# Kernel tuning notes

Hardware: AMD Instinct MI355X
Metric: run time of the kernel (lower is better)

Reference implementation:

```python
import jax, jax.numpy as jnp
import numpy as np

B, NS, NT = 8, 1024, 1024
SRC, TGT, OUT, H = 1024, 1024, 1024, 8
DH = OUT // H  # per-head dim = 128


def setup_inputs() -> dict:
    key = jax.random.key(0)
    ks = jax.random.split(key, 9)
    s = 0.02
    return {
        "src": jax.random.normal(ks[0], (B, NS, SRC), jnp.float32),
        "tgt": jax.random.normal(ks[1], (B, NT, TGT), jnp.float32),
        "src_mask": jnp.ones((B, NS), jnp.float32),
        "tgt_mask": jnp.ones((B, NT), jnp.float32),
        "Ws": jax.random.normal(ks[2], (2 * OUT, SRC), jnp.float32) * s,
        "bs": jnp.zeros((2 * OUT,), jnp.float32),
        "Wt": jax.random.normal(ks[3], (OUT, TGT), jnp.float32) * s,
        "bt": jnp.zeros((OUT,), jnp.float32),
        "Wo": jax.random.normal(ks[4], (OUT, OUT + TGT), jnp.float32) * s,
        "bo": jnp.zeros((OUT,), jnp.float32),
    }


def reference(src, tgt, src_mask, tgt_mask, Ws, bs, Wt, bt, Wo, bo):
    # src_lin / tgt_lin (FCNet = linear, no activation, drop=0 at eval)
    src_trans = jnp.einsum("bsf,of->bso", src, Ws) + bs  # [B,NS,2*OUT]
    tgt_trans = jnp.einsum("btf,of->bto", tgt, Wt) + bt  # [B,NT,OUT]
    src_trans = src_trans * src_mask[:, :, None]
    tgt_trans = tgt_trans * tgt_mask[:, :, None]

    src_key, src_val = jnp.split(src_trans, 2, axis=2)  # each [B,NS,OUT]
    # head split along channels == reshape to [.., H, DH]
    k = src_key.reshape(B, NS, H, DH)
    v = src_val.reshape(B, NS, H, DH)
    q = tgt_trans.reshape(B, NT, H, DH)

    scores = jnp.einsum("bthd,bshd->bhts", q, k) / jnp.sqrt(jnp.float32(DH))
    scores = jnp.where(src_mask[:, None, None, :] == 0, -jnp.inf, scores)
    attn = jax.nn.softmax(scores, axis=-1)  # [B,H,NT,NS]
    tgt_update = jnp.einsum("bhts,bshd->bthd", attn, v).reshape(B, NT, OUT)

    cat_tgt = jnp.concatenate([tgt, tgt_update], axis=2)  # [B,NT,TGT+OUT]
    update_tgt = jnp.einsum("btf,of->bto", cat_tgt, Wo) + bo
    return update_tgt
```

## Files before the change

kernel.cpp:

```cpp
#include <hip/hip_runtime.h>


typedef __bf16 bf16x8 __attribute__((ext_vector_type(8)));
typedef float f32x4 __attribute__((ext_vector_type(4)));
typedef unsigned short u16;
typedef unsigned short u16x8 __attribute__((ext_vector_type(8)));

#define MFMA16(a, b, c) __builtin_amdgcn_mfma_f32_16x16x32_bf16((a), (b), (c), 0, 0, 0)

__device__ __forceinline__ float bf2f(u16 b) {
  return __uint_as_float(((unsigned)b) << 16);
}
__device__ __forceinline__ u16 f2bf(float f) {
  unsigned u = __float_as_uint(f);
  u += 0x7fffu + ((u >> 16) & 1u);
  return (u16)(u >> 16);
}
__device__ __forceinline__ u16 f2bf_hw(float f) {
  __bf16 h = (__bf16)f;
  return __builtin_bit_cast(u16, h);
}

__device__ __forceinline__ void async16(const u16* g, u16* l) {
  __builtin_amdgcn_global_load_lds(
      (const __attribute__((address_space(1))) unsigned int*)g,
      (__attribute__((address_space(3))) unsigned int*)l, 16, 0, 0);
}

struct Cvt5 {
  const float* src[5];
  unsigned cnt4[5];
  unsigned ooff[5];
};

__global__ __launch_bounds__(256)
void cvt5_kernel(Cvt5 a, u16* __restrict__ out, unsigned total4)
{
  unsigned gid = blockIdx.x * 256u + threadIdx.x;
  if (gid >= total4) return;
  unsigned rem = gid;
  int s = 0;
  while (s < 4 && rem >= a.cnt4[s]) { rem -= a.cnt4[s]; ++s; }
  const float4 v = ((const float4*)a.src[s])[rem];
  ushort4 o;
  o.x = f2bf(v.x); o.y = f2bf(v.y); o.z = f2bf(v.z); o.w = f2bf(v.w);
  *(ushort4*)(out + a.ooff[s] + (size_t)rem * 4) = o;
}

__global__ __launch_bounds__(256, 3)
void gemm12_kernel(const u16* __restrict__ srcb, const u16* __restrict__ tgtb,
                   const u16* __restrict__ Wsb, const u16* __restrict__ Wtb,
                   const float* __restrict__ bs, const float* __restrict__ bt,
                   const float* __restrict__ smask, const float* __restrict__ tmask,
                   u16* __restrict__ kvbuf, u16* __restrict__ qbuf)
{
  __shared__ u16 smem[16384];
  u16* As = smem;
  u16* Bs = smem + 8192;

  const int tid  = threadIdx.x;
  const int lane = tid & 63;
  const int w    = tid >> 6;
  const int wm = w >> 1, wn = w & 1;
  const int quad = lane >> 4, lr = lane & 15;

  const unsigned nwg  = gridDim.x * gridDim.y;
  const unsigned wgid = blockIdx.y * gridDim.x + blockIdx.x;
  const unsigned swz  = (wgid & 7u) * (nwg >> 3) + (wgid >> 3);
  const int nt = (int)(swz % gridDim.x);
  const int mt = (int)(swz / gridDim.x);
  const int m0 = mt * 128;
  const int n0 = nt * 128;

  const bool isQ = (n0 >= 2048);
  const u16* Ap = isQ ? tgtb : srcb;
  const u16* Bp = isQ ? (Wtb + (size_t)(n0 - 2048) * 1024)
                      : (Wsb + (size_t)n0 * 1024);
  const float* bias = isQ ? (bt + (n0 - 2048)) : (bs + n0);
  const float* rsc  = isQ ? tmask : smask;

  const f32x4 z4 = {0.f, 0.f, 0.f, 0.f};
  f32x4 acc[4][4];
#pragma unroll
  for (int i = 0; i < 4; ++i)
#pragma unroll
    for (int j = 0; j < 4; ++j)
      acc[i][j] = z4;

  const int acolsw = (((tid & 7) ^ ((tid >> 3) & 7)) * 8);
  const int ssw = lr & 7;

  for (int k0 = 0; k0 < 1024; k0 += 64) {
    __syncthreads();
#pragma unroll
    for (int it = 0; it < 4; ++it) {
      const int row = it * 32 + (tid >> 3);
      const int ldsbase = (it * 256 + (tid & 192)) * 8;
      async16(Ap + (size_t)(m0 + row) * 1024 + (k0 + acolsw), &As[ldsbase]);
      async16(Bp + (size_t)row * 1024        + (k0 + acolsw), &Bs[ldsbase]);
    }
    __syncthreads();

#pragma unroll
    for (int kk = 0; kk < 2; ++kk) {
      const int rc = (((kk << 2) | quad) ^ ssw) * 8;
      bf16x8 af[4], bfr[4];
#pragma unroll
      for (int i = 0; i < 4; ++i)
        af[i] = *(const bf16x8*)&As[(wm * 64 + i * 16 + lr) * 64 + rc];
#pragma unroll
      for (int j = 0; j < 4; ++j)
        bfr[j] = *(const bf16x8*)&Bs[(wn * 64 + j * 16 + lr) * 64 + rc];
#pragma unroll
      for (int i = 0; i < 4; ++i)
#pragma unroll
        for (int j = 0; j < 4; ++j)
          acc[i][j] = MFMA16(af[i], bfr[j], acc[i][j]);
    }
  }

  float bv[4];
#pragma unroll
  for (int j = 0; j < 4; ++j)
    bv[j] = bias[wn * 64 + j * 16 + lr];

  if (isQ) {
    const int c0 = n0 - 2048;
#pragma unroll
    for (int i = 0; i < 4; ++i)
#pragma unroll
      for (int r = 0; r < 4; ++r) {
        const int grow = m0 + wm * 64 + i * 16 + quad * 4 + r;
        const float rs = rsc[grow];
#pragma unroll
        for (int j = 0; j < 4; ++j) {
          const int gcol = c0 + wn * 64 + j * 16 + lr;
          qbuf[(size_t)grow * 1024 + gcol] = f2bf_hw((acc[i][j][r] + bv[j]) * rs);
        }
      }
  } else {
    u16* kvtile = smem;
    __syncthreads();

    const int bb  = m0 >> 10;
    const int s0b = m0 & 1023;
    const bool isK = (n0 < 1024);
    const int h = (isK ? n0 : n0 - 1024) >> 7;
    const size_t bh = (size_t)(bb * 8 + h);

#pragma unroll
    for (int i = 0; i < 4; ++i)
#pragma unroll
      for (int r = 0; r < 4; ++r) {
        const int sl = wm * 64 + i * 16 + quad * 4 + r;
        const float rs = rsc[m0 + sl];
#pragma unroll
        for (int j = 0; j < 4; ++j) {
          const int d = wn * 64 + j * 16 + lr;
          const float val = (acc[i][j][r] + bv[j]) * rs;
          int c, e;
          if (isK) {
            c = (d >> 3) * 128 + sl;
            c ^= ((c >> 2) & 2) ^ ((c >> 7) & 1);
            e = d & 7;
          } else {
            c = (sl >> 6) * 1024 + (((sl >> 3) & 7) * 128) + d;
            c ^= (c >> 7) & 1;
            e = sl & 7;
          }
          kvtile[c * 8 + e] = f2bf_hw(val);
        }
      }
    __syncthreads();

    const size_t gbase = isK
        ? (bh * 131072 + (size_t)s0b * 8)
        : ((size_t)8388608 + bh * 131072 + (size_t)(s0b >> 6) * 8192);
#pragma unroll
    for (int it = 0; it < 8; ++it) {
      const int idx = it * 256 + tid;
      int lc;
      size_t dst;
      if (isK) {
        lc  = idx ^ ((idx >> 2) & 2) ^ ((idx >> 7) & 1);
        dst = gbase + (size_t)(idx >> 7) * 8192 + (size_t)(idx & 127) * 8;
      } else {
        lc  = idx ^ ((idx >> 7) & 1);
        dst = gbase + (size_t)idx * 8;
      }
      *(u16x8*)(kvbuf + dst) = *(const u16x8*)&kvtile[lc * 8];
    }
  }
}

__global__ __launch_bounds__(256, 3)
void gemm3_kernel(const u16* __restrict__ A0, const u16* __restrict__ A1,
                  const u16* __restrict__ Bw, const float* __restrict__ bias,
                  float* __restrict__ C)
{
  __shared__ u16 As[128 * 64];
  __shared__ u16 Bs[128 * 64];
  const int tid  = threadIdx.x;
  const int lane = tid & 63;
  const int w    = tid >> 6;
  const int wm = w >> 1, wn = w & 1;
  const int quad = lane >> 4, lr = lane & 15;
  const unsigned nwg  = gridDim.x * gridDim.y;
  const unsigned wgid = blockIdx.y * gridDim.x + blockIdx.x;
  const unsigned swz  = (wgid & 7u) * (nwg >> 3) + (wgid >> 3);
  const int m0 = (int)(swz / gridDim.x) * 128;
  const int n0 = (int)(swz % gridDim.x) * 128;

  const f32x4 z4 = {0.f, 0.f, 0.f, 0.f};
  f32x4 acc[4][4];
#pragma unroll
  for (int i = 0; i < 4; ++i)
#pragma unroll
    for (int j = 0; j < 4; ++j)
      acc[i][j] = z4;

  const int acolsw = (((tid & 7) ^ ((tid >> 3) & 7)) * 8);
  const int ssw = lr & 7;

  auto kstep = [&](const u16* Ap, int kk0, int k0) {
    __syncthreads();
#pragma unroll
    for (int it = 0; it < 4; ++it) {
      const int row = it * 32 + (tid >> 3);
      const int ldsbase = (it * 256 + (tid & 192)) * 8;
      async16(Ap + (size_t)(m0 + row) * 1024 + (kk0 + acolsw), &As[ldsbase]);
      async16(Bw + (size_t)(n0 + row) * 2048 + (k0 + acolsw), &Bs[ldsbase]);
    }
    __syncthreads();

#pragma unroll
    for (int kk = 0; kk < 2; ++kk) {
      const int rc = (((kk << 2) | quad) ^ ssw) * 8;
      bf16x8 af[4], bfr[4];
#pragma unroll
      for (int i = 0; i < 4; ++i)
        af[i] = *(const bf16x8*)&As[(wm * 64 + i * 16 + lr) * 64 + rc];
#pragma unroll
      for (int j = 0; j < 4; ++j)
        bfr[j] = *(const bf16x8*)&Bs[(wn * 64 + j * 16 + lr) * 64 + rc];
#pragma unroll
      for (int i = 0; i < 4; ++i)
#pragma unroll
        for (int j = 0; j < 4; ++j)
          acc[i][j] = MFMA16(af[i], bfr[j], acc[i][j]);
    }
  };

  for (int k0 = 0; k0 < 1024; k0 += 64) kstep(A0, k0, k0);
  for (int k0 = 1024; k0 < 2048; k0 += 64) kstep(A1, k0 - 1024, k0);

  float bv[4];
#pragma unroll
  for (int j = 0; j < 4; ++j)
    bv[j] = bias[n0 + wn * 64 + j * 16 + lr];

#pragma unroll
  for (int i = 0; i < 4; ++i)
#pragma unroll
    for (int r = 0; r < 4; ++r) {
      const int grow = m0 + wm * 64 + i * 16 + quad * 4 + r;
#pragma unroll
      for (int j = 0; j < 4; ++j) {
        const int gcol = n0 + wn * 64 + j * 16 + lr;
        C[(size_t)grow * 1024 + gcol] = acc[i][j][r] + bv[j];
      }
    }
}

#define SCLOG2E 0.12751813754618667f

__global__ __launch_bounds__(256, 2)
void flash_kernel(const u16* __restrict__ q, const u16* __restrict__ Kg,
                  const u16* __restrict__ Vg,
                  const float* __restrict__ smask, u16* __restrict__ upd)
{
  __shared__ u16 Ks[2][64 * 128];
  __shared__ u16 Vs[2][64 * 128];
  __shared__ u16 Ps[4][2 * 16 * 64];

  const int tid  = threadIdx.x;
  const int lane = tid & 63;
  const int w    = tid >> 6;
  const int quad = lane >> 4, lr = lane & 15;
  const int bh_i = blockIdx.x;
  const int qt   = blockIdx.y;
  const int b = bh_i >> 3, h = bh_i & 7;
  const size_t bh = (size_t)bh_i;

  const size_t qrow0 = (size_t)b * 1024 + qt * 128 + w * 16;

  bf16x8 qf[2][4];
#pragma unroll
  for (int s = 0; s < 2; ++s)
#pragma unroll
    for (int kk = 0; kk < 4; ++kk)
      qf[s][kk] = *(const bf16x8*)
          &q[(qrow0 + s * 64 + lr) * 1024 + h * 128 + kk * 32 + quad * 8];

  unsigned long long mbits = 0ull;
#pragma unroll
  for (int t = 0; t < 16; ++t)
#pragma unroll
    for (int j = 0; j < 4; ++j) {
      const float mv = smask[b * 1024 + t * 64 + j * 16 + lr];
      if (mv == 0.f) mbits |= (1ull << (t * 4 + j));
    }

  auto stage = [&](int t, int bb) {
    const int s0 = t * 64;
#pragma unroll
    for (int it = 0; it < 4; ++it) {
      const int dc = it * 4 + w;
      async16(Kg + (((bh * 16 + dc) * 1024) + s0 + lane) * 8,
              &Ks[bb][(it * 256 + (tid & 192)) * 8]);
    }
#pragma unroll
    for (int it = 0; it < 4; ++it) {
      async16(Vg + ((bh * 16 + t) * 1024 + it * 256 + tid) * 8,
              &Vs[bb][(it * 256 + (tid & 192)) * 8]);
    }
  };

  const f32x4 z4 = {0.f, 0.f, 0.f, 0.f};
  f32x4 oacc[2][8];
#pragma unroll
  for (int s = 0; s < 2; ++s)
#pragma unroll
    for (int jd = 0; jd < 8; ++jd) oacc[s][jd] = z4;
  float lsum[2][4] = {{0.f, 0.f, 0.f, 0.f}, {0.f, 0.f, 0.f, 0.f}};

  stage(0, 0);
  stage(1, 1);

#pragma unroll 1
  for (int t = 0; t < 16; ++t) {
    const int bb = t & 1;
    asm volatile("s_waitcnt vmcnt(8)" ::: "memory");
    __builtin_amdgcn_s_barrier();

    float mb[4];
#pragma unroll
    for (int j = 0; j < 4; ++j)
      mb[j] = ((mbits >> (t * 4 + j)) & 1ull) ? -1e30f : 0.f;

    f32x4 sacc[2][4];
#pragma unroll
    for (int s = 0; s < 2; ++s)
#pragma unroll
      for (int j = 0; j < 4; ++j) sacc[s][j] = z4;
    __builtin_amdgcn_s_setprio(1);
#pragma unroll
    for (int kk = 0; kk < 4; ++kk) {
      bf16x8 kb[4];
#pragma unroll
      for (int j = 0; j < 4; ++j)
        kb[j] = *(const bf16x8*)&Ks[bb][((kk * 4 + quad) * 64 + j * 16 + lr) * 8];
#pragma unroll
      for (int s = 0; s < 2; ++s)
#pragma unroll
        for (int j = 0; j < 4; ++j)
          sacc[s][j] = MFMA16(qf[s][kk], kb[j], sacc[s][j]);
    }
    __builtin_amdgcn_s_setprio(0);

#pragma unroll
    for (int s = 0; s < 2; ++s)
#pragma unroll
      for (int r = 0; r < 4; ++r) {
        const int row = quad * 4 + r;
        const int rsw = (row & 7) * 8;
        float ps = 0.f;
#pragma unroll
        for (int j = 0; j < 4; ++j) {
          const float p = exp2f(fmaf(sacc[s][j][r], SCLOG2E, mb[j]));
          ps += p;
          Ps[w][s * 1024 + row * 64 + ((j * 16 + lr) ^ rsw)] = f2bf_hw(p);
        }
        lsum[s][r] += ps;
      }

    __builtin_amdgcn_s_setprio(1);
#pragma unroll
    for (int kk2 = 0; kk2 < 2; ++kk2) {
      bf16x8 pa[2], vb[8];
#pragma unroll
      for (int s = 0; s < 2; ++s)
        pa[s] = *(const bf16x8*)
            &Ps[w][s * 1024 + lr * 64 + ((kk2 * 32 + quad * 8) ^ ((lr & 7) * 8))];
#pragma unroll
      for (int jd = 0; jd < 8; ++jd)
        vb[jd] = *(const bf16x8*)&Vs[bb][((kk2 * 4 + quad) * 128 + jd * 16 + lr) * 8];
#pragma unroll
      for (int s = 0; s < 2; ++s)
#pragma unroll
        for (int jd = 0; jd < 8; ++jd)
          oacc[s][jd] = MFMA16(pa[s], vb[jd], oacc[s][jd]);
    }
    __builtin_amdgcn_s_setprio(0);

    __builtin_amdgcn_s_barrier();
    stage((t + 2) & 15, bb);
  }

  asm volatile("s_waitcnt vmcnt(0)" ::: "memory");

#pragma unroll
  for (int s = 0; s < 2; ++s)
#pragma unroll
    for (int r = 0; r < 4; ++r) {
      float l = lsum[s][r];
      l += __shfl_xor(l, 1);
      l += __shfl_xor(l, 2);
      l += __shfl_xor(l, 4);
      l += __shfl_xor(l, 8);
      const float inv = 1.f / l;
      const size_t grow = qrow0 + s * 64 + quad * 4 + r;
#pragma unroll
      for (int jd = 0; jd < 8; ++jd)
        upd[grow * 1024 + h * 128 + jd * 16 + lr] = f2bf_hw(oacc[s][jd][r] * inv);
    }
}

__global__ void magic_kernel(float* out, float val)
{
  if (threadIdx.x == 0 && blockIdx.x == 0) out[0] = val;
}

extern "C" void kernel_launch(void* const* d_in, const int* in_sizes, int n_in,
                              void* d_out, int out_size, void* d_ws, size_t ws_size,
                              hipStream_t stream)
{
  static const int dict_sz[10]   = {8388608, 8388608, 8192, 8192, 2097152,
                                    2048, 1048576, 1024, 2097152, 1024};
  static const int sorted_sz[10] = {2097152, 2097152, 1048576, 1024, 2048,
                                    1024, 8388608, 8192, 8388608, 8192};
  bool is_dict = (n_in == 10), is_sorted = (n_in == 10);
  if (n_in == 10) {
    for (int i = 0; i < 10; ++i) {
      if (in_sizes[i] != dict_sz[i])   is_dict = false;
      if (in_sizes[i] != sorted_sz[i]) is_sorted = false;
    }
  }

  const float *src, *tgt, *smask, *tmask, *Ws, *bs, *Wt, *bt, *Wo, *bo;
  if (is_sorted) {
    Wo    = (const float*)d_in[0];
    Ws    = (const float*)d_in[1];
    Wt    = (const float*)d_in[2];
    bo    = (const float*)d_in[3];
    bs    = (const float*)d_in[4];
    bt    = (const float*)d_in[5];
    src   = (const float*)d_in[6];
    smask = (const float*)d_in[7];
    tgt   = (const float*)d_in[8];
    tmask = (const float*)d_in[9];
  } else {
    src   = (const float*)d_in[0];
    tgt   = (const float*)d_in[1];
    smask = (const float*)d_in[2];
    tmask = (const float*)d_in[3];
    Ws    = (const float*)d_in[4];
    bs    = (const float*)d_in[5];
    Wt    = (const float*)d_in[6];
    bt    = (const float*)d_in[7];
    Wo    = (const float*)d_in[8];
    bo    = (const float*)d_in[9];
  }
  float* out = (float*)d_out;

  const size_t KV = 16777216, Q = 8388608, UPD = 8388608;
  const unsigned segsz[5] = {8388608u, 8388608u, 2097152u, 1048576u, 2097152u};
  size_t total_u16 = KV + Q + UPD;
  unsigned aoff[5], off = 0, total4 = 0;
  for (int i = 0; i < 5; ++i) {
    aoff[i] = off;
    off += segsz[i];
    total4 += segsz[i] / 4u;
  }
  total_u16 += off;

  unsigned ws_mb = (unsigned)(ws_size >> 20);
  if (ws_mb > 999u) ws_mb = 999u;
  if (!is_dict && !is_sorted) {
    magic_kernel<<<dim3(1), dim3(64), 0, stream>>>(out, 4000.f + (float)ws_mb);
    return;
  }
  if (ws_size < total_u16 * 2) {
    magic_kernel<<<dim3(1), dim3(64), 0, stream>>>(out, 3000.f + (float)ws_mb);
    return;
  }

  u16* kvbuf  = (u16*)d_ws;
  u16* qbuf   = kvbuf + KV;
  u16* updbuf = qbuf + Q;
  u16* arena  = updbuf + UPD;

  Cvt5 ca;
  const float* segp[5] = {src, tgt, Ws, Wt, Wo};
  for (int i = 0; i < 5; ++i) {
    ca.src[i]  = segp[i];
    ca.cnt4[i] = segsz[i] / 4u;
    ca.ooff[i] = aoff[i];
  }
  const u16* srcb = arena + aoff[0];
  const u16* tgtb = arena + aoff[1];
  const u16* Wsb  = arena + aoff[2];
  const u16* Wtb  = arena + aoff[3];
  const u16* Wob  = arena + aoff[4];

  dim3 blk(256);
  cvt5_kernel<<<dim3((total4 + 255u) / 256u), blk, 0, stream>>>(ca, arena, total4);
  gemm12_kernel<<<dim3(24, 64), blk, 0, stream>>>(
      srcb, tgtb, Wsb, Wtb, bs, bt, smask, tmask, kvbuf, qbuf);
  flash_kernel<<<dim3(64, 8), blk, 0, stream>>>(
      qbuf, kvbuf, kvbuf + 8388608, smask, updbuf);
  gemm3_kernel<<<dim3(8, 64), blk, 0, stream>>>(
      tgtb, updbuf, Wob, bo, out);
}
```

Measured before the change: 300.8 us.

## Overlap tgt half of output GEMM with attention in one heterogeneous launch

```diff
diff --git a/kernel.cpp b/kernel.cpp
--- a/kernel.cpp
+++ b/kernel.cpp
@@ -193,10 +193,236 @@
   }
 }
 
+#define SCLOG2E 0.12751813754618667f
+
+__global__ __launch_bounds__(256, 2)
+void fused_fg_kernel(const u16* __restrict__ q, const u16* __restrict__ Kg,
+                     const u16* __restrict__ Vg, const float* __restrict__ smask,
+                     u16* __restrict__ upd,
+                     const u16* __restrict__ tgtb, const u16* __restrict__ Wob,
+                     const float* __restrict__ bo, float* __restrict__ out)
+{
+  __shared__ u16 smem[40960];
+  const int tid  = threadIdx.x;
+  const int lane = tid & 63;
+  const int w    = tid >> 6;
+  const int quad = lane >> 4, lr = lane & 15;
+  const unsigned id  = blockIdx.x;
+  const unsigned sub = ((id >> 4) << 3) | (id & 7u);
+  const f32x4 z4 = {0.f, 0.f, 0.f, 0.f};
+
+  if (((id >> 3) & 1u) == 0u) {
+    u16* Ksm = smem;
+    u16* Vsm = smem + 16384;
+    u16* Psm = smem + 32768;
+    const int bh_i = (int)(sub & 63u);
+    const int qt   = (int)(sub >> 6);
+    const int b = bh_i >> 3, h = bh_i & 7;
+    const size_t bh = (size_t)bh_i;
+
+    const size_t qrow0 = (size_t)b * 1024 + qt * 128 + w * 16;
+
+    bf16x8 qf[2][4];
+#pragma unroll
+    for (int s = 0; s < 2; ++s)
+#pragma unroll
+      for (int kk = 0; kk < 4; ++kk)
+        qf[s][kk] = *(const bf16x8*)
+            &q[(qrow0 + s * 64 + lr) * 1024 + h * 128 + kk * 32 + quad * 8];
+
+    unsigned long long mbits = 0ull;
+#pragma unroll
+    for (int t = 0; t < 16; ++t)
+#pragma unroll
+      for (int j = 0; j < 4; ++j) {
+        const float mv = smask[b * 1024 + t * 64 + j * 16 + lr];
+        if (mv == 0.f) mbits |= (1ull << (t * 4 + j));
+      }
+
+    auto stage = [&](int t, int bb) {
+      const int s0 = t * 64;
+#pragma unroll
+      for (int it = 0; it < 4; ++it) {
+        const int dc = it * 4 + w;
+        async16(Kg + (((bh * 16 + dc) * 1024) + s0 + lane) * 8,
+                Ksm + bb * 8192 + (it * 256 + (tid & 192)) * 8);
+      }
+#pragma unroll
+      for (int it = 0; it < 4; ++it) {
+        async16(Vg + ((bh * 16 + t) * 1024 + it * 256 + tid) * 8,
+                Vsm + bb * 8192 + (it * 256 + (tid & 192)) * 8);
+      }
+    };
+
+    f32x4 oacc[2][8];
+#pragma unroll
+    for (int s = 0; s < 2; ++s)
+#pragma unroll
+      for (int jd = 0; jd < 8; ++jd) oacc[s][jd] = z4;
+    float lsum[2][4] = {{0.f, 0.f, 0.f, 0.f}, {0.f, 0.f, 0.f, 0.f}};
+
+    stage(0, 0);
+    stage(1, 1);
+
+#pragma unroll 1
+    for (int t = 0; t < 16; ++t) {
+      const int bb = t & 1;
+      asm volatile("s_waitcnt vmcnt(8)" ::: "memory");
+      __builtin_amdgcn_s_barrier();
+
+      float mb[4];
+#pragma unroll
+      for (int j = 0; j < 4; ++j)
+        mb[j] = ((mbits >> (t * 4 + j)) & 1ull) ? -1e30f : 0.f;
+
+      f32x4 sacc[2][4];
+#pragma unroll
+      for (int s = 0; s < 2; ++s)
+#pragma unroll
+        for (int j = 0; j < 4; ++j) sacc[s][j] = z4;
+      __builtin_amdgcn_s_setprio(1);
+#pragma unroll
+      for (int kk = 0; kk < 4; ++kk) {
+        bf16x8 kb[4];
+#pragma unroll
+        for (int j = 0; j < 4; ++j)
+          kb[j] = *(const bf16x8*)
+              &Ksm[bb * 8192 + ((kk * 4 + quad) * 64 + j * 16 + lr) * 8];
+#pragma unroll
+        for (int s = 0; s < 2; ++s)
+#pragma unroll
+          for (int j = 0; j < 4; ++j)
+            sacc[s][j] = MFMA16(qf[s][kk], kb[j], sacc[s][j]);
+      }
+      __builtin_amdgcn_s_setprio(0);
+
+#pragma unroll
+      for (int s = 0; s < 2; ++s)
+#pragma unroll
+        for (int r = 0; r < 4; ++r) {
+          const int row = quad * 4 + r;
+          const int rsw = (row & 7) * 8;
+          float ps = 0.f;
+#pragma unroll
+          for (int j = 0; j < 4; ++j) {
+            const float p = exp2f(fmaf(sacc[s][j][r], SCLOG2E, mb[j]));
+            ps += p;
+            Psm[w * 2048 + s * 1024 + row * 64 + ((j * 16 + lr) ^ rsw)] = f2bf_hw(p);
+          }
+          lsum[s][r] += ps;
+        }
+
+      __builtin_amdgcn_s_setprio(1);
+#pragma unroll
+      for (int kk2 = 0; kk2 < 2; ++kk2) {
+        bf16x8 pa[2], vb[8];
+#pragma unroll
+        for (int s = 0; s < 2; ++s)
+          pa[s] = *(const bf16x8*)
+              &Psm[w * 2048 + s * 1024 + lr * 64 +
+                   ((kk2 * 32 + quad * 8) ^ ((lr & 7) * 8))];
+#pragma unroll
+        for (int jd = 0; jd < 8; ++jd)
+          vb[jd] = *(const bf16x8*)
+              &Vsm[bb * 8192 + ((kk2 * 4 + quad) * 128 + jd * 16 + lr) * 8];
+#pragma unroll
+        for (int s = 0; s < 2; ++s)
+#pragma unroll
+          for (int jd = 0; jd < 8; ++jd)
+            oacc[s][jd] = MFMA16(pa[s], vb[jd], oacc[s][jd]);
+      }
+      __builtin_amdgcn_s_setprio(0);
+
+      __builtin_amdgcn_s_barrier();
+      stage((t + 2) & 15, bb);
+    }
+
+    asm volatile("s_waitcnt vmcnt(0)" ::: "memory");
+
+#pragma unroll
+    for (int s = 0; s < 2; ++s)
+#pragma unroll
+      for (int r = 0; r < 4; ++r) {
+        float l = lsum[s][r];
+        l += __shfl_xor(l, 1);
+        l += __shfl_xor(l, 2);
+        l += __shfl_xor(l, 4);
+        l += __shfl_xor(l, 8);
+        const float inv = 1.f / l;
+        const size_t grow = qrow0 + s * 64 + quad * 4 + r;
+#pragma unroll
+        for (int jd = 0; jd < 8; ++jd)
+          upd[grow * 1024 + h * 128 + jd * 16 + lr] = f2bf_hw(oacc[s][jd][r] * inv);
+      }
+  } else {
+    u16* As = smem;
+    u16* Bs = smem + 8192;
+    const int wm = w >> 1, wn = w & 1;
+    const unsigned lid = (sub & 7u) * 64u + (sub >> 3);
+    const int m0 = (int)(lid >> 3) * 128;
+    const int n0 = (int)(lid & 7u) * 128;
+
+    f32x4 acc[4][4];
+#pragma unroll
+    for (int i = 0; i < 4; ++i)
+#pragma unroll
+      for (int j = 0; j < 4; ++j)
+        acc[i][j] = z4;
+
+    const int acolsw = (((tid & 7) ^ ((tid >> 3) & 7)) * 8);
+    const int ssw = lr & 7;
+
+    for (int k0 = 0; k0 < 1024; k0 += 64) {
+      __syncthreads();
+#pragma unroll
+      for (int it = 0; it < 4; ++it) {
+        const int row = it * 32 + (tid >> 3);
+        const int ldsbase = (it * 256 + (tid & 192)) * 8;
+        async16(tgtb + (size_t)(m0 + row) * 1024 + (k0 + acolsw), &As[ldsbase]);
+        async16(Wob + (size_t)(n0 + row) * 2048 + (k0 + acolsw), &Bs[ldsbase]);
+      }
+      __syncthreads();
+
+#pragma unroll
+      for (int kk = 0; kk < 2; ++kk) {
+        const int rc = (((kk << 2) | quad) ^ ssw) * 8;
+        bf16x8 af[4], bfr[4];
+#pragma unroll
+        for (int i = 0; i < 4; ++i)
+          af[i] = *(const bf16x8*)&As[(wm * 64 + i * 16 + lr) * 64 + rc];
+#pragma unroll
+        for (int j = 0; j < 4; ++j)
+          bfr[j] = *(const bf16x8*)&Bs[(wn * 64 + j * 16 + lr) * 64 + rc];
+#pragma unroll
+        for (int i = 0; i < 4; ++i)
+#pragma unroll
+          for (int j = 0; j < 4; ++j)
+            acc[i][j] = MFMA16(af[i], bfr[j], acc[i][j]);
+      }
+    }
+
+    float bv[4];
+#pragma unroll
+    for (int j = 0; j < 4; ++j)
+      bv[j] = bo[n0 + wn * 64 + j * 16 + lr];
+
+#pragma unroll
+    for (int i = 0; i < 4; ++i)
+#pragma unroll
+      for (int r = 0; r < 4; ++r) {
+        const int grow = m0 + wm * 64 + i * 16 + quad * 4 + r;
+#pragma unroll
+        for (int j = 0; j < 4; ++j) {
+          const int gcol = n0 + wn * 64 + j * 16 + lr;
+          out[(size_t)grow * 1024 + gcol] = acc[i][j][r] + bv[j];
+        }
+      }
+  }
+}
+
 __global__ __launch_bounds__(256, 3)
-void gemm3_kernel(const u16* __restrict__ A0, const u16* __restrict__ A1,
-                  const u16* __restrict__ Bw, const float* __restrict__ bias,
-                  float* __restrict__ C)
+void gemm3b_kernel(const u16* __restrict__ A0, const u16* __restrict__ Bw,
+                   float* __restrict__ C)
 {
   __shared__ u16 As[128 * 64];
   __shared__ u16 Bs[128 * 64];
@@ -222,14 +448,14 @@
   const int acolsw = (((tid & 7) ^ ((tid >> 3) & 7)) * 8);
   const int ssw = lr & 7;
 
-  auto kstep = [&](const u16* Ap, int kk0, int k0) {
+  for (int k0 = 0; k0 < 1024; k0 += 64) {
     __syncthreads();
 #pragma unroll
     for (int it = 0; it < 4; ++it) {
       const int row = it * 32 + (tid >> 3);
       const int ldsbase = (it * 256 + (tid & 192)) * 8;
-      async16(Ap + (size_t)(m0 + row) * 1024 + (kk0 + acolsw), &As[ldsbase]);
-      async16(Bw + (size_t)(n0 + row) * 2048 + (k0 + acolsw), &Bs[ldsbase]);
+      async16(A0 + (size_t)(m0 + row) * 1024 + (k0 + acolsw), &As[ldsbase]);
+      async16(Bw + (size_t)(n0 + row) * 2048 + (1024 + k0 + acolsw), &Bs[ldsbase]);
     }
     __syncthreads();
 
@@ -249,15 +475,7 @@
         for (int j = 0; j < 4; ++j)
           acc[i][j] = MFMA16(af[i], bfr[j], acc[i][j]);
     }
-  };
-
-  for (int k0 = 0; k0 < 1024; k0 += 64) kstep(A0, k0, k0);
-  for (int k0 = 1024; k0 < 2048; k0 += 64) kstep(A1, k0 - 1024, k0);
-
-  float bv[4];
-#pragma unroll
-  for (int j = 0; j < 4; ++j)
-    bv[j] = bias[n0 + wn * 64 + j * 16 + lr];
+  }
 
 #pragma unroll
   for (int i = 0; i < 4; ++i)
@@ -267,162 +485,9 @@
 #pragma unroll
       for (int j = 0; j < 4; ++j) {
         const int gcol = n0 + wn * 64 + j * 16 + lr;
-        C[(size_t)grow * 1024 + gcol] = acc[i][j][r] + bv[j];
-      }
-    }
-}
-
-#define SCLOG2E 0.12751813754618667f
-
-__global__ __launch_bounds__(256, 2)
-void flash_kernel(const u16* __restrict__ q, const u16* __restrict__ Kg,
-                  const u16* __restrict__ Vg,
-                  const float* __restrict__ smask, u16* __restrict__ upd)
-{
-  __shared__ u16 Ks[2][64 * 128];
-  __shared__ u16 Vs[2][64 * 128];
-  __shared__ u16 Ps[4][2 * 16 * 64];
-
-  const int tid  = threadIdx.x;
-  const int lane = tid & 63;
-  const int w    = tid >> 6;
-  const int quad = lane >> 4, lr = lane & 15;
-  const int bh_i = blockIdx.x;
-  const int qt   = blockIdx.y;
-  const int b = bh_i >> 3, h = bh_i & 7;
-  const size_t bh = (size_t)bh_i;
-
-  const size_t qrow0 = (size_t)b * 1024 + qt * 128 + w * 16;
-
-  bf16x8 qf[2][4];
-#pragma unroll
-  for (int s = 0; s < 2; ++s)
-#pragma unroll
-    for (int kk = 0; kk < 4; ++kk)
-      qf[s][kk] = *(const bf16x8*)
-          &q[(qrow0 + s * 64 + lr) * 1024 + h * 128 + kk * 32 + quad * 8];
-
-  unsigned long long mbits = 0ull;
-#pragma unroll
-  for (int t = 0; t < 16; ++t)
-#pragma unroll
-    for (int j = 0; j < 4; ++j) {
-      const float mv = smask[b * 1024 + t * 64 + j * 16 + lr];
-      if (mv == 0.f) mbits |= (1ull << (t * 4 + j));
-    }
-
-  auto stage = [&](int t, int bb) {
-    const int s0 = t * 64;
-#pragma unroll
-    for (int it = 0; it < 4; ++it) {
-      const int dc = it * 4 + w;
-      async16(Kg + (((bh * 16 + dc) * 1024) + s0 + lane) * 8,
-              &Ks[bb][(it * 256 + (tid & 192)) * 8]);
-    }
-#pragma unroll
-    for (int it = 0; it < 4; ++it) {
-      async16(Vg + ((bh * 16 + t) * 1024 + it * 256 + tid) * 8,
-              &Vs[bb][(it * 256 + (tid & 192)) * 8]);
-    }
-  };
-
-  const f32x4 z4 = {0.f, 0.f, 0.f, 0.f};
-  f32x4 oacc[2][8];
-#pragma unroll
-  for (int s = 0; s < 2; ++s)
-#pragma unroll
-    for (int jd = 0; jd < 8; ++jd) oacc[s][jd] = z4;
-  float lsum[2][4] = {{0.f, 0.f, 0.f, 0.f}, {0.f, 0.f, 0.f, 0.f}};
-
-  stage(0, 0);
-  stage(1, 1);
-
-#pragma unroll 1
-  for (int t = 0; t < 16; ++t) {
-    const int bb = t & 1;
-    asm volatile("s_waitcnt vmcnt(8)" ::: "memory");
-    __builtin_amdgcn_s_barrier();
-
-    float mb[4];
-#pragma unroll
-    for (int j = 0; j < 4; ++j)
-      mb[j] = ((mbits >> (t * 4 + j)) & 1ull) ? -1e30f : 0.f;
-
-    f32x4 sacc[2][4];
-#pragma unroll
-    for (int s = 0; s < 2; ++s)
-#pragma unroll
-      for (int j = 0; j < 4; ++j) sacc[s][j] = z4;
-    __builtin_amdgcn_s_setprio(1);
-#pragma unroll
-    for (int kk = 0; kk < 4; ++kk) {
-      bf16x8 kb[4];
-#pragma unroll
-      for (int j = 0; j < 4; ++j)
-        kb[j] = *(const bf16x8*)&Ks[bb][((kk * 4 + quad) * 64 + j * 16 + lr) * 8];
-#pragma unroll
-      for (int s = 0; s < 2; ++s)
-#pragma unroll
-        for (int j = 0; j < 4; ++j)
-          sacc[s][j] = MFMA16(qf[s][kk], kb[j], sacc[s][j]);
-    }
-    __builtin_amdgcn_s_setprio(0);
-
-#pragma unroll
-    for (int s = 0; s < 2; ++s)
-#pragma unroll
-      for (int r = 0; r < 4; ++r) {
-        const int row = quad * 4 + r;
-        const int rsw = (row & 7) * 8;
-        float ps = 0.f;
-#pragma unroll
-        for (int j = 0; j < 4; ++j) {
-          const float p = exp2f(fmaf(sacc[s][j][r], SCLOG2E, mb[j]));
-          ps += p;
-          Ps[w][s * 1024 + row * 64 + ((j * 16 + lr) ^ rsw)] = f2bf_hw(p);
-        }
-        lsum[s][r] += ps;
-      }
-
-    __builtin_amdgcn_s_setprio(1);
-#pragma unroll
-    for (int kk2 = 0; kk2 < 2; ++kk2) {
-      bf16x8 pa[2], vb[8];
-#pragma unroll
-      for (int s = 0; s < 2; ++s)
-        pa[s] = *(const bf16x8*)
-            &Ps[w][s * 1024 + lr * 64 + ((kk2 * 32 + quad * 8) ^ ((lr & 7) * 8))];
-#pragma unroll
-      for (int jd = 0; jd < 8; ++jd)
-        vb[jd] = *(const bf16x8*)&Vs[bb][((kk2 * 4 + quad) * 128 + jd * 16 + lr) * 8];
-#pragma unroll
-      for (int s = 0; s < 2; ++s)
-#pragma unroll
-        for (int jd = 0; jd < 8; ++jd)
-          oacc[s][jd] = MFMA16(pa[s], vb[jd], oacc[s][jd]);
-    }
-    __builtin_amdgcn_s_setprio(0);
-
-    __builtin_amdgcn_s_barrier();
-    stage((t + 2) & 15, bb);
-  }
-
-  asm volatile("s_waitcnt vmcnt(0)" ::: "memory");
-
-#pragma unroll
-  for (int s = 0; s < 2; ++s)
-#pragma unroll
-    for (int r = 0; r < 4; ++r) {
-      float l = lsum[s][r];
-      l += __shfl_xor(l, 1);
-      l += __shfl_xor(l, 2);
-      l += __shfl_xor(l, 4);
-      l += __shfl_xor(l, 8);
-      const float inv = 1.f / l;
-      const size_t grow = qrow0 + s * 64 + quad * 4 + r;
-#pragma unroll
-      for (int jd = 0; jd < 8; ++jd)
-        upd[grow * 1024 + h * 128 + jd * 16 + lr] = f2bf_hw(oacc[s][jd][r] * inv);
+        const size_t idx = (size_t)grow * 1024 + gcol;
+        C[idx] = C[idx] + acc[i][j][r];
+      }
     }
 }
 
@@ -517,8 +582,7 @@
   cvt5_kernel<<<dim3((total4 + 255u) / 256u), blk, 0, stream>>>(ca, arena, total4);
   gemm12_kernel<<<dim3(24, 64), blk, 0, stream>>>(
       srcb, tgtb, Wsb, Wtb, bs, bt, smask, tmask, kvbuf, qbuf);
-  flash_kernel<<<dim3(64, 8), blk, 0, stream>>>(
-      qbuf, kvbuf, kvbuf + 8388608, smask, updbuf);
-  gemm3_kernel<<<dim3(8, 64), blk, 0, stream>>>(
-      tgtb, updbuf, Wob, bo, out);
-}
+  fused_fg_kernel<<<dim3(1024), blk, 0, stream>>>(
+      qbuf, kvbuf, kvbuf + 8388608, smask, updbuf, tgtb, Wob, bo, out);
+  gemm3b_kernel<<<dim3(8, 64), blk, 0, stream>>>(updbuf, Wob, out);
+}
```

Result: slower. 338.1 us (+12.4%).
